# Optimization experiments

Hardware: AMD Instinct MI355X
Metric: run time of the kernel (lower is better)

Reference implementation:

```python
import jax, jax.numpy as jnp
import numpy as np


def setup_inputs() -> dict:
    key = jax.random.key(0)
    ks = jax.random.split(key, 6)
    B, C, H, W, K = 4, 64, 352, 1216, 3
    OC = K * K - 1  # 8 guide channels from convbn
    return {
        "feature": jax.random.normal(ks[0], (B, C, H, W), jnp.float32),
        "conv_w": jax.random.normal(ks[1], (OC, C, 3, 3), jnp.float32) * 0.05,
        "gamma": jax.random.uniform(ks[2], (OC,), jnp.float32, 0.5, 1.5),
        "beta": jax.random.normal(ks[3], (OC,), jnp.float32) * 0.1,
        "mean": jax.random.normal(ks[4], (OC,), jnp.float32) * 0.1,
        "var": jax.random.uniform(ks[5], (OC,), jnp.float32, 0.5, 1.5),
        "kernel_size": K,
    }


def reference(feature, conv_w, gamma, beta, mean, var, kernel_size):
    k = kernel_size
    eps = 1e-5
    # conv 3x3, stride 1, pad 1, no bias  -> [B, k*k-1, H, W]
    x = jax.lax.conv_general_dilated(
        feature, conv_w, window_strides=(1, 1), padding=((1, 1), (1, 1)),
        dimension_numbers=("NCHW", "OIHW", "NCHW"))
    c = lambda v: v[None, :, None, None]
    # BatchNorm2d in eval mode (running stats + affine)
    guide = (x - c(mean)) * (c(gamma) * jax.lax.rsqrt(c(var) + eps)) + c(beta)
    # L1-normalize across channels, middle weight = 1 - sum of the others
    gsum = jnp.sum(jnp.abs(guide), axis=1, keepdims=True)
    guide = guide / gsum
    guide_mid = 1.0 - jnp.sum(guide, axis=1, keepdims=True)
    mid = (k * k - 1) // 2
    # per-offset zero-pad each single channel into [H+k-1, W+k-1] canvas
    pads = []
    for t in range(k * k):  # fixed small loop over kernel offsets (k*k = 9)
        i, j = t // k, t % k  # top=i, bottom=k-1-i, left=j, right=k-1-j
        if t < mid:
            ch = guide[:, t:t + 1]
        elif t > mid:
            ch = guide[:, t - 1:t]
        else:
            ch = guide_mid
        pads.append(jnp.pad(ch, ((0, 0), (0, 0), (i, k - 1 - i), (j, k - 1 - j))))
    return jnp.concatenate(pads, axis=1)  # [B, k*k, H+k-1, W+k-1]
```

## Files before the change

### kernel.cpp

```cpp
#include <hip/hip_runtime.h>
#include <hip/hip_bf16.h>

#define BATCH 4
#define CIN 64
#define HH 352
#define WW 1216
#define OCH 8
#define OHH 354
#define OWW 1218
#define HW (HH * WW)

#define BH 16
#define BW 32
#define FR 18
#define FC 34
#define NPOS (FR * FC)
#define NTHR 256
#define NTASK (NPOS * 4)
#define NIT 10

typedef short bf16x8 __attribute__((ext_vector_type(8)));
typedef float f32x4  __attribute__((ext_vector_type(4)));

static __device__ __forceinline__ unsigned f2bf(float x) {
    unsigned u = __float_as_uint(x);
    return (u + 0x7FFFu + ((u >> 16) & 1u)) >> 16;
}

__global__ void repack_kernel(const float* __restrict__ conv_w,
                              const float* __restrict__ gamma,
                              const float* __restrict__ beta,
                              const float* __restrict__ mean,
                              const float* __restrict__ var,
                              unsigned short* __restrict__ wB,
                              float* __restrict__ bias)
{
    int tid = blockIdx.x * 256 + threadIdx.x;
    if (tid < 18 * 64) {
        int tc = tid >> 6;
        int lane = tid & 63;
        int tap = tc >> 1, cc = tc & 1;
        int oc = lane & 15, hi = lane >> 4;
        unsigned v[8];
#pragma unroll
        for (int j = 0; j < 8; ++j) {
            float w = 0.f;
            if (oc < 8) {
                int c = cc * 32 + hi * 8 + j;
                float scl = gamma[oc] * rsqrtf(var[oc] + 1e-5f);
                w = conv_w[((size_t)oc * CIN + c) * 9 + tap] * scl;
            }
            v[j] = f2bf(w);
        }
        uint4 pk;
        pk.x = v[0] | (v[1] << 16);
        pk.y = v[2] | (v[3] << 16);
        pk.z = v[4] | (v[5] << 16);
        pk.w = v[6] | (v[7] << 16);
        ((uint4*)wB)[tid] = pk;
    }
    if (tid < OCH) {
        float scl = gamma[tid] * rsqrtf(var[tid] + 1e-5f);
        bias[tid] = beta[tid] - mean[tid] * scl;
    }
}

__global__ void border_kernel(float* __restrict__ out)
{
    const int bt = blockIdx.x;
    const int t = bt % 9;
    const int i = t / 3, j = t % 3;
    float* pl = out + (size_t)bt * OHH * OWW;
    const int r0 = (i == 0) ? HH : 0;
    const int r1 = (i == 2) ? 1 : (OHH - 1);
    const int c0 = (j == 0) ? WW : 0;
    const int c1 = (j == 2) ? 1 : (OWW - 1);
    const int nrow = 2 * OWW;
    for (int idx = threadIdx.x; idx < 2 * OWW + 2 * OHH; idx += blockDim.x) {
        if (idx < nrow) {
            int r = (idx < OWW) ? r0 : r1;
            int c = (idx < OWW) ? idx : idx - OWW;
            pl[(size_t)r * OWW + c] = 0.f;
        } else {
            int k = idx - nrow;
            int c = (k < OHH) ? c0 : c1;
            int r = (k < OHH) ? k : k - OHH;
            pl[(size_t)r * OWW + c] = 0.f;
        }
    }
}

__global__ __launch_bounds__(NTHR, 2)
void conv_mfma(const float* __restrict__ feature,
               const unsigned short* __restrict__ wB,
               const float* __restrict__ bias,
               float* __restrict__ out)
{
    __shared__ uint4 sF[NPOS * 4];

    const int tid  = threadIdx.x;
    const int wave = tid >> 6;
    const int lane = tid & 63;
    const int oc   = lane & 15;
    const int hi   = lane >> 4;
    const int b  = blockIdx.z;
    const int h0 = blockIdx.y * BH;
    const int w0 = blockIdx.x * BW;

    const float* fb = feature + (size_t)b * CIN * HW;

    const int soct = tid & 3;
    const int p0   = tid >> 2;

    f32x4 acc[4][2];
#pragma unroll
    for (int rr = 0; rr < 4; ++rr)
#pragma unroll
        for (int cg = 0; cg < 2; ++cg) acc[rr][cg] = (f32x4)0.f;

#pragma unroll 1
    for (int cc = 0; cc < 2; ++cc) {
        if (cc) __syncthreads();

        const float* chbase = fb + (size_t)(cc * 32 + soct * 8) * HW;
        float v[NIT][8];
        float msk[NIT];
        int   cps[NIT];
#pragma unroll
        for (int it = 0; it < NIT; ++it) {
            int pos = p0 + it * 64;
            int cp = (pos < NPOS) ? pos : (NPOS - 1);
            int fr = cp / FC;
            int fc = cp - fr * FC;
            int gh = h0 - 1 + fr, gw = w0 - 1 + fc;
            bool ok = ((unsigned)gh < (unsigned)HH) && ((unsigned)gw < (unsigned)WW);
            int sgh = min(max(gh, 0), HH - 1);
            int sgw = min(max(gw, 0), WW - 1);
            const float* sp = chbase + sgh * WW + sgw;
#pragma unroll
            for (int j = 0; j < 8; ++j) v[it][j] = sp[(size_t)j * HW];
            msk[it] = ok ? 1.f : 0.f;
            cps[it] = cp;
        }
        bf16x8 bw[9];
#pragma unroll
        for (int t = 0; t < 9; ++t)
            bw[t] = ((const bf16x8*)wB)[(t * 2 + cc) * 64 + lane];
#pragma unroll
        for (int it = 0; it < NIT; ++it) {
            float mk = msk[it];
            uint4 pk;
            pk.x = f2bf(v[it][0] * mk) | (f2bf(v[it][1] * mk) << 16);
            pk.y = f2bf(v[it][2] * mk) | (f2bf(v[it][3] * mk) << 16);
            pk.z = f2bf(v[it][4] * mk) | (f2bf(v[it][5] * mk) << 16);
            pk.w = f2bf(v[it][6] * mk) | (f2bf(v[it][7] * mk) << 16);
            int cp = cps[it];
            sF[cp * 4 + (soct ^ ((cp >> 1) & 3))] = pk;
        }
        __syncthreads();

#pragma unroll
        for (int t = 0; t < 9; ++t) {
            const int dh = t / 3, dw = t % 3;
#pragma unroll
            for (int rr = 0; rr < 4; ++rr) {
                const int fr = wave * 4 + rr + dh;
#pragma unroll
                for (int cg = 0; cg < 2; ++cg) {
                    const int fc = cg * 16 + oc + dw;
                    const int pp = fr * FC + fc;
                    bf16x8 av = *reinterpret_cast<const bf16x8*>(&sF[pp * 4 + (hi ^ ((pp >> 1) & 3))]);
                    acc[rr][cg] = __builtin_amdgcn_mfma_f32_16x16x32_bf16(av, bw[t], acc[rr][cg], 0, 0, 0);
                }
            }
        }
    }

    const float myb = (oc < 8) ? bias[oc] : 0.f;
    const int t = (oc < 8) ? ((oc < 4) ? oc : oc + 1) : 4;
    const bool dow = (oc <= 8);
    const int ii = t / 3, jj = t % 3;
    float* pl = out + ((size_t)(b * 9 + t) * OHH + ii) * OWW + jj;

#pragma unroll
    for (int rr = 0; rr < 4; ++rr) {
        const int h = h0 + wave * 4 + rr;
#pragma unroll
        for (int cg = 0; cg < 2; ++cg) {
#pragma unroll
            for (int reg = 0; reg < 4; ++reg) {
                float v = acc[rr][cg][reg] + myb;
                float av = fabsf(v);
                float sv = v;
                av += __shfl_xor(av, 1);  sv += __shfl_xor(sv, 1);
                av += __shfl_xor(av, 2);  sv += __shfl_xor(sv, 2);
                av += __shfl_xor(av, 4);  sv += __shfl_xor(sv, 4);
                av += __shfl_xor(av, 8);  sv += __shfl_xor(sv, 8);
                float inv = 1.0f / av;
                float val = (oc == 8) ? (1.0f - sv * inv) : (v * inv);
                if (dow) {
                    int w = w0 + cg * 16 + hi * 4 + reg;
                    pl[(size_t)h * OWW + w] = val;
                }
            }
        }
    }
}

extern "C" void kernel_launch(void* const* d_in, const int* in_sizes, int n_in,
                              void* d_out, int out_size, void* d_ws, size_t ws_size,
                              hipStream_t stream) {
    const float* feature = (const float*)d_in[0];
    const float* conv_w  = (const float*)d_in[1];
    const float* gamma   = (const float*)d_in[2];
    const float* beta    = (const float*)d_in[3];
    const float* mean    = (const float*)d_in[4];
    const float* var     = (const float*)d_in[5];
    float* out = (float*)d_out;
    unsigned short* wB = (unsigned short*)d_ws;
    float* bias = (float*)((char*)d_ws + 18432);

    border_kernel<<<BATCH * 9, 256, 0, stream>>>(out);
    repack_kernel<<<5, 256, 0, stream>>>(conv_w, gamma, beta, mean, var, wB, bias);

    dim3 grid(WW / BW, HH / BH, BATCH);
    conv_mfma<<<grid, NTHR, 0, stream>>>(feature, wB, bias, out);
}
```

Before: 261.0 us.

## Pre-transpose feature to padded NHWC bf16 and read conv operands directly

Adds a transpose kernel that converts the NCHW fp32 feature map into a zero-padded NHWC bf16 buffer in workspace, plus a ring kernel that zeroes the padding border. The conv kernel then loads MFMA A operands straight from global memory as contiguous 16-byte channel vectors. This removes the LDS staging, the per-position masking and the strided per-channel loads. The cost is an extra full pass over the input (read fp32, write bf16) and dependence on workspace size; if the workspace is too small, the old path runs instead.

```diff
diff --git a/kernel.cpp b/kernel.cpp
--- a/kernel.cpp
+++ b/kernel.cpp
@@ -9,6 +9,8 @@
 #define OHH 354
 #define OWW 1218
 #define HW (HH * WW)
+#define HP 354
+#define WP 1218
 
 #define BH 16
 #define BW 32
@@ -16,8 +18,8 @@
 #define FC 34
 #define NPOS (FR * FC)
 #define NTHR 256
-#define NTASK (NPOS * 4)
 #define NIT 10
+#define NRING 3140
 
 typedef short bf16x8 __attribute__((ext_vector_type(8)));
 typedef float f32x4  __attribute__((ext_vector_type(4)));
@@ -90,14 +92,60 @@
     }
 }
 
+__global__ void ring_kernel(unsigned short* __restrict__ ft)
+{
+    int idx = blockIdx.x * 256 + threadIdx.x;
+    if (idx >= BATCH * NRING * 8) return;
+    int q = idx & 7;
+    int pp = idx >> 3;
+    int b = pp / NRING;
+    int r = pp - b * NRING;
+    int hp, wp;
+    if (r < WP)            { hp = 0;               wp = r; }
+    else if (r < 2 * WP)   { hp = HP - 1;          wp = r - WP; }
+    else if (r < 2 * WP + HH) { hp = 1 + (r - 2 * WP);      wp = 0; }
+    else                   { hp = 1 + (r - 2 * WP - HH);    wp = WP - 1; }
+    uint4 z; z.x = 0; z.y = 0; z.z = 0; z.w = 0;
+    *(uint4*)(ft + ((((size_t)b * HP + hp) * WP + wp) * 64 + q * 8)) = z;
+}
+
+__global__ __launch_bounds__(256, 2)
+void transpose_kernel(const float* __restrict__ feature,
+                      unsigned short* __restrict__ ft)
+{
+    __shared__ unsigned short sT[64 * 72];
+    const int tid = threadIdx.x;
+    const int tx = tid & 15, ty = tid >> 4;
+    const int w0 = blockIdx.x * 64;
+    const int h  = blockIdx.y;
+    const int b  = blockIdx.z;
+
+    const float* fb = feature + (size_t)b * CIN * HW + (size_t)h * WW + w0;
+#pragma unroll
+    for (int i = 0; i < 4; ++i) {
+        int ch = ty + i * 16;
+        float4 v = *(const float4*)(fb + (size_t)ch * HW + tx * 4);
+        int px = tx * 4;
+        sT[(px + 0) * 72 + ch] = (unsigned short)f2bf(v.x);
+        sT[(px + 1) * 72 + ch] = (unsigned short)f2bf(v.y);
+        sT[(px + 2) * 72 + ch] = (unsigned short)f2bf(v.z);
+        sT[(px + 3) * 72 + ch] = (unsigned short)f2bf(v.w);
+    }
+    __syncthreads();
+    const int pix = tid >> 2, q = tid & 3;
+    const uint4* src = (const uint4*)(sT + pix * 72 + q * 16);
+    unsigned short* dst = ft + ((((size_t)b * HP + (h + 1)) * WP + (w0 + pix + 1)) * 64 + q * 16);
+    uint4 a0 = src[0], a1 = src[1];
+    ((uint4*)dst)[0] = a0;
+    ((uint4*)dst)[1] = a1;
+}
+
 __global__ __launch_bounds__(NTHR, 2)
-void conv_mfma(const float* __restrict__ feature,
+void conv_nhwc(const unsigned short* __restrict__ ft,
                const unsigned short* __restrict__ wB,
                const float* __restrict__ bias,
                float* __restrict__ out)
 {
-    __shared__ uint4 sF[NPOS * 4];
-
     const int tid  = threadIdx.x;
     const int wave = tid >> 6;
     const int lane = tid & 63;
@@ -107,10 +155,10 @@
     const int h0 = blockIdx.y * BH;
     const int w0 = blockIdx.x * BW;
 
-    const float* fb = feature + (size_t)b * CIN * HW;
-
-    const int soct = tid & 3;
-    const int p0   = tid >> 2;
+    bf16x8 bw[18];
+#pragma unroll
+    for (int k = 0; k < 18; ++k)
+        bw[k] = ((const bf16x8*)wB)[k * 64 + lane];
 
     f32x4 acc[4][2];
 #pragma unroll
@@ -118,59 +166,22 @@
 #pragma unroll
         for (int cg = 0; cg < 2; ++cg) acc[rr][cg] = (f32x4)0.f;
 
-#pragma unroll 1
-    for (int cc = 0; cc < 2; ++cc) {
-        if (cc) __syncthreads();
-
-        const float* chbase = fb + (size_t)(cc * 32 + soct * 8) * HW;
-        float v[NIT][8];
-        float msk[NIT];
-        int   cps[NIT];
-#pragma unroll
-        for (int it = 0; it < NIT; ++it) {
-            int pos = p0 + it * 64;
-            int cp = (pos < NPOS) ? pos : (NPOS - 1);
-            int fr = cp / FC;
-            int fc = cp - fr * FC;
-            int gh = h0 - 1 + fr, gw = w0 - 1 + fc;
-            bool ok = ((unsigned)gh < (unsigned)HH) && ((unsigned)gw < (unsigned)WW);
-            int sgh = min(max(gh, 0), HH - 1);
-            int sgw = min(max(gw, 0), WW - 1);
-            const float* sp = chbase + sgh * WW + sgw;
-#pragma unroll
-            for (int j = 0; j < 8; ++j) v[it][j] = sp[(size_t)j * HW];
-            msk[it] = ok ? 1.f : 0.f;
-            cps[it] = cp;
-        }
-        bf16x8 bw[9];
-#pragma unroll
-        for (int t = 0; t < 9; ++t)
-            bw[t] = ((const bf16x8*)wB)[(t * 2 + cc) * 64 + lane];
-#pragma unroll
-        for (int it = 0; it < NIT; ++it) {
-            float mk = msk[it];
-            uint4 pk;
-            pk.x = f2bf(v[it][0] * mk) | (f2bf(v[it][1] * mk) << 16);
-            pk.y = f2bf(v[it][2] * mk) | (f2bf(v[it][3] * mk) << 16);
-            pk.z = f2bf(v[it][4] * mk) | (f2bf(v[it][5] * mk) << 16);
-            pk.w = f2bf(v[it][6] * mk) | (f2bf(v[it][7] * mk) << 16);
-            int cp = cps[it];
-            sF[cp * 4 + (soct ^ ((cp >> 1) & 3))] = pk;
-        }
-        __syncthreads();
-
+    const unsigned short* fbase = ft + (size_t)b * HP * WP * 64 + hi * 8;
+
+#pragma unroll
+    for (int rr = 0; rr < 4; ++rr) {
+        const int hrow = h0 + wave * 4 + rr;
 #pragma unroll
         for (int t = 0; t < 9; ++t) {
             const int dh = t / 3, dw = t % 3;
 #pragma unroll
-            for (int rr = 0; rr < 4; ++rr) {
-                const int fr = wave * 4 + rr + dh;
-#pragma unroll
-                for (int cg = 0; cg < 2; ++cg) {
-                    const int fc = cg * 16 + oc + dw;
-                    const int pp = fr * FC + fc;
-                    bf16x8 av = *reinterpret_cast<const bf16x8*>(&sF[pp * 4 + (hi ^ ((pp >> 1) & 3))]);
-                    acc[rr][cg] = __builtin_amdgcn_mfma_f32_16x16x32_bf16(av, bw[t], acc[rr][cg], 0, 0, 0);
+            for (int cg = 0; cg < 2; ++cg) {
+                const unsigned short* p =
+                    fbase + ((size_t)(hrow + dh) * WP + (w0 + oc + dw + cg * 16)) * 64;
+#pragma unroll
+                for (int cc = 0; cc < 2; ++cc) {
+                    bf16x8 av = *(const bf16x8*)(p + cc * 32);
+                    acc[rr][cg] = __builtin_amdgcn_mfma_f32_16x16x32_bf16(av, bw[t * 2 + cc], acc[rr][cg], 0, 0, 0);
                 }
             }
         }
@@ -207,6 +218,120 @@
     }
 }
 
+__global__ __launch_bounds__(NTHR, 2)
+void conv_mfma(const float* __restrict__ feature,
+               const unsigned short* __restrict__ wB,
+               const float* __restrict__ bias,
+               float* __restrict__ out)
+{
+    __shared__ uint4 sF[NPOS * 4];
+
+    const int tid  = threadIdx.x;
+    const int wave = tid >> 6;
+    const int lane = tid & 63;
+    const int oc   = lane & 15;
+    const int hi   = lane >> 4;
+    const int b  = blockIdx.z;
+    const int h0 = blockIdx.y * BH;
+    const int w0 = blockIdx.x * BW;
+
+    const float* fb = feature + (size_t)b * CIN * HW;
+    const int soct = tid & 3;
+    const int p0   = tid >> 2;
+
+    f32x4 acc[4][2];
+#pragma unroll
+    for (int rr = 0; rr < 4; ++rr)
+#pragma unroll
+        for (int cg = 0; cg < 2; ++cg) acc[rr][cg] = (f32x4)0.f;
+
+#pragma unroll 1
+    for (int cc = 0; cc < 2; ++cc) {
+        if (cc) __syncthreads();
+        const float* chbase = fb + (size_t)(cc * 32 + soct * 8) * HW;
+        float v[NIT][8];
+        float msk[NIT];
+        int   cps[NIT];
+#pragma unroll
+        for (int it = 0; it < NIT; ++it) {
+            int pos = p0 + it * 64;
+            int cp = (pos < NPOS) ? pos : (NPOS - 1);
+            int fr = cp / FC;
+            int fc = cp - fr * FC;
+            int gh = h0 - 1 + fr, gw = w0 - 1 + fc;
+            bool ok = ((unsigned)gh < (unsigned)HH) && ((unsigned)gw < (unsigned)WW);
+            int sgh = min(max(gh, 0), HH - 1);
+            int sgw = min(max(gw, 0), WW - 1);
+            const float* sp = chbase + sgh * WW + sgw;
+#pragma unroll
+            for (int j = 0; j < 8; ++j) v[it][j] = sp[(size_t)j * HW];
+            msk[it] = ok ? 1.f : 0.f;
+            cps[it] = cp;
+        }
+        bf16x8 bwl[9];
+#pragma unroll
+        for (int t = 0; t < 9; ++t)
+            bwl[t] = ((const bf16x8*)wB)[(t * 2 + cc) * 64 + lane];
+#pragma unroll
+        for (int it = 0; it < NIT; ++it) {
+            float mk = msk[it];
+            uint4 pk;
+            pk.x = f2bf(v[it][0] * mk) | (f2bf(v[it][1] * mk) << 16);
+            pk.y = f2bf(v[it][2] * mk) | (f2bf(v[it][3] * mk) << 16);
+            pk.z = f2bf(v[it][4] * mk) | (f2bf(v[it][5] * mk) << 16);
+            pk.w = f2bf(v[it][6] * mk) | (f2bf(v[it][7] * mk) << 16);
+            int cp = cps[it];
+            sF[cp * 4 + (soct ^ ((cp >> 1) & 3))] = pk;
+        }
+        __syncthreads();
+#pragma unroll
+        for (int t = 0; t < 9; ++t) {
+            const int dh = t / 3, dw = t % 3;
+#pragma unroll
+            for (int rr = 0; rr < 4; ++rr) {
+                const int fr = wave * 4 + rr + dh;
+#pragma unroll
+                for (int cg = 0; cg < 2; ++cg) {
+                    const int fc = cg * 16 + oc + dw;
+                    const int pp = fr * FC + fc;
+                    bf16x8 av = *reinterpret_cast<const bf16x8*>(&sF[pp * 4 + (hi ^ ((pp >> 1) & 3))]);
+                    acc[rr][cg] = __builtin_amdgcn_mfma_f32_16x16x32_bf16(av, bwl[t], acc[rr][cg], 0, 0, 0);
+                }
+            }
+        }
+    }
+
+    const float myb = (oc < 8) ? bias[oc] : 0.f;
+    const int t = (oc < 8) ? ((oc < 4) ? oc : oc + 1) : 4;
+    const bool dow = (oc <= 8);
+    const int ii = t / 3, jj = t % 3;
+    float* pl = out + ((size_t)(b * 9 + t) * OHH + ii) * OWW + jj;
+
+#pragma unroll
+    for (int rr = 0; rr < 4; ++rr) {
+        const int h = h0 + wave * 4 + rr;
+#pragma unroll
+        for (int cg = 0; cg < 2; ++cg) {
+#pragma unroll
+            for (int reg = 0; reg < 4; ++reg) {
+                float v = acc[rr][cg][reg] + myb;
+                float av = fabsf(v);
+                float sv = v;
+                av += __shfl_xor(av, 1);  sv += __shfl_xor(sv, 1);
+                av += __shfl_xor(av, 2);  sv += __shfl_xor(sv, 2);
+                av += __shfl_xor(av, 4);  sv += __shfl_xor(sv, 4);
+                av += __shfl_xor(av, 8);  sv += __shfl_xor(sv, 8);
+                float inv = 1.0f / av;
+                float val = (oc == 8) ? (1.0f - sv * inv) : (v * inv);
+                if (dow) {
+                    int w = w0 + cg * 16 + hi * 4 + reg;
+                    pl[(size_t)h * OWW + w] = val;
+                }
+            }
+        }
+    }
+}
+
 extern "C" void kernel_launch(void* const* d_in, const int* in_sizes, int n_in,
                               void* d_out, int out_size, void* d_ws, size_t ws_size,
                               hipStream_t stream) {
@@ -217,12 +342,23 @@
     const float* mean    = (const float*)d_in[4];
     const float* var     = (const float*)d_in[5];
     float* out = (float*)d_out;
+
     unsigned short* wB = (unsigned short*)d_ws;
     float* bias = (float*)((char*)d_ws + 18432);
+    unsigned short* ft = (unsigned short*)((char*)d_ws + 32768);
+    const size_t ft_bytes = (size_t)BATCH * HP * WP * 64 * 2;
+    const size_t need = 32768 + ft_bytes;
 
     border_kernel<<<BATCH * 9, 256, 0, stream>>>(out);
     repack_kernel<<<5, 256, 0, stream>>>(conv_w, gamma, beta, mean, var, wB, bias);
 
     dim3 grid(WW / BW, HH / BH, BATCH);
-    conv_mfma<<<grid, NTHR, 0, stream>>>(feature, wB, bias, out);
-}
+
+    if (ws_size >= need) {
+        ring_kernel<<<(BATCH * NRING * 8 + 255) / 256, 256, 0, stream>>>(ft);
+        transpose_kernel<<<dim3(WW / 64, HH, BATCH), 256, 0, stream>>>(feature, ft);
+        conv_nhwc<<<grid, NTHR, 0, stream>>>(ft, wB, bias, out);
+    } else {
+        conv_mfma<<<grid, NTHR, 0, stream>>>(feature, wB, bias, out);
+    }
+}
```

Measured after the change: 326.5 us. 1.25x slower.

## Double-buffer channel chunks in LDS and remap blocks across XCDs

Applied to the files above, without the earlier changes.

Splits the shared-memory tile into two buffers so the global loads for the second 32-channel chunk are issued before the MFMA work on the first chunk, overlapping memory latency with compute. All 18 weight fragments and the per-position offsets and masks are computed once up front. The 3D grid becomes a 1D grid with a remapping that gives each XCD a contiguous range of tiles, aiming to improve L2 locality for the halo rows. Costs are doubled LDS per block and more registers, which may reduce occupancy.

```diff
diff --git a/kernel.cpp b/kernel.cpp
--- a/kernel.cpp
+++ b/kernel.cpp
@@ -16,8 +16,11 @@
 #define FC 34
 #define NPOS (FR * FC)
 #define NTHR 256
-#define NTASK (NPOS * 4)
 #define NIT 10
+#define GX 38
+#define GY 22
+#define NWG (GX * GY * BATCH)
+#define CPX (NWG / 8)
 
 typedef short bf16x8 __attribute__((ext_vector_type(8)));
 typedef float f32x4  __attribute__((ext_vector_type(4)));
@@ -90,91 +93,104 @@
     }
 }
 
+#define ISSUE(VB, CC) { \
+    const float* chb = fb + (size_t)((CC) * 32 + soct * 8) * HW; \
+    _Pragma("unroll") for (int it = 0; it < NIT; ++it) { \
+        const float* sp = chb + off[it]; \
+        _Pragma("unroll") for (int j = 0; j < 8; ++j) VB[it][j] = sp[(size_t)j * HW]; \
+    } }
+
+#define PACK(VB, BUF) { \
+    _Pragma("unroll") for (int it = 0; it < NIT; ++it) { \
+        float mk = msk[it]; \
+        uint4 pk; \
+        pk.x = f2bf(VB[it][0] * mk) | (f2bf(VB[it][1] * mk) << 16); \
+        pk.y = f2bf(VB[it][2] * mk) | (f2bf(VB[it][3] * mk) << 16); \
+        pk.z = f2bf(VB[it][4] * mk) | (f2bf(VB[it][5] * mk) << 16); \
+        pk.w = f2bf(VB[it][6] * mk) | (f2bf(VB[it][7] * mk) << 16); \
+        (BUF)[slot[it]] = pk; \
+    } }
+
+#define MFMA_CHUNK(BUF, CC) \
+    _Pragma("unroll") for (int t = 0; t < 9; ++t) { \
+        const int dh = t / 3, dw = t % 3; \
+        _Pragma("unroll") for (int rr = 0; rr < 4; ++rr) { \
+            const int frq = wv4 + rr + dh; \
+            _Pragma("unroll") for (int cg = 0; cg < 2; ++cg) { \
+                const int fcq = cg * 16 + oc + dw; \
+                const int pp = frq * FC + fcq; \
+                bf16x8 av = *reinterpret_cast<const bf16x8*>(&(BUF)[pp * 4 + (hi ^ ((pp >> 1) & 3))]); \
+                acc[rr][cg] = __builtin_amdgcn_mfma_f32_16x16x32_bf16(av, bw[t * 2 + (CC)], acc[rr][cg], 0, 0, 0); \
+            } } }
+
 __global__ __launch_bounds__(NTHR, 2)
 void conv_mfma(const float* __restrict__ feature,
                const unsigned short* __restrict__ wB,
                const float* __restrict__ bias,
                float* __restrict__ out)
 {
-    __shared__ uint4 sF[NPOS * 4];
+    __shared__ uint4 sA[NPOS * 4];
+    __shared__ uint4 sB[NPOS * 4];
+
+    const int lin = blockIdx.x;
+    const int wg  = (lin & 7) * CPX + (lin >> 3);
+    const int bx  = wg % GX;
+    const int byz = wg / GX;
+    const int by  = byz % GY;
+    const int b   = byz / GY;
 
     const int tid  = threadIdx.x;
     const int wave = tid >> 6;
     const int lane = tid & 63;
     const int oc   = lane & 15;
     const int hi   = lane >> 4;
-    const int b  = blockIdx.z;
-    const int h0 = blockIdx.y * BH;
-    const int w0 = blockIdx.x * BW;
+    const int wv4  = wave * 4;
+    const int h0 = by * BH;
+    const int w0 = bx * BW;
 
     const float* fb = feature + (size_t)b * CIN * HW;
-
     const int soct = tid & 3;
     const int p0   = tid >> 2;
 
+    int   off[NIT], slot[NIT];
+    float msk[NIT];
+#pragma unroll
+    for (int it = 0; it < NIT; ++it) {
+        int pos = p0 + it * 64;
+        int cp = (pos < NPOS) ? pos : (NPOS - 1);
+        int fr = cp / FC;
+        int fc = cp - fr * FC;
+        int gh = h0 - 1 + fr, gw = w0 - 1 + fc;
+        bool ok = ((unsigned)gh < (unsigned)HH) && ((unsigned)gw < (unsigned)WW);
+        int sgh = min(max(gh, 0), HH - 1);
+        int sgw = min(max(gw, 0), WW - 1);
+        off[it]  = sgh * WW + sgw;
+        msk[it]  = ok ? 1.f : 0.f;
+        slot[it] = cp * 4 + (soct ^ ((cp >> 1) & 3));
+    }
+
     f32x4 acc[4][2];
 #pragma unroll
     for (int rr = 0; rr < 4; ++rr)
 #pragma unroll
         for (int cg = 0; cg < 2; ++cg) acc[rr][cg] = (f32x4)0.f;
 
-#pragma unroll 1
-    for (int cc = 0; cc < 2; ++cc) {
-        if (cc) __syncthreads();
-
-        const float* chbase = fb + (size_t)(cc * 32 + soct * 8) * HW;
-        float v[NIT][8];
-        float msk[NIT];
-        int   cps[NIT];
-#pragma unroll
-        for (int it = 0; it < NIT; ++it) {
-            int pos = p0 + it * 64;
-            int cp = (pos < NPOS) ? pos : (NPOS - 1);
-            int fr = cp / FC;
-            int fc = cp - fr * FC;
-            int gh = h0 - 1 + fr, gw = w0 - 1 + fc;
-            bool ok = ((unsigned)gh < (unsigned)HH) && ((unsigned)gw < (unsigned)WW);
-            int sgh = min(max(gh, 0), HH - 1);
-            int sgw = min(max(gw, 0), WW - 1);
-            const float* sp = chbase + sgh * WW + sgw;
-#pragma unroll
-            for (int j = 0; j < 8; ++j) v[it][j] = sp[(size_t)j * HW];
-            msk[it] = ok ? 1.f : 0.f;
-            cps[it] = cp;
-        }
-        bf16x8 bw[9];
-#pragma unroll
-        for (int t = 0; t < 9; ++t)
-            bw[t] = ((const bf16x8*)wB)[(t * 2 + cc) * 64 + lane];
-#pragma unroll
-        for (int it = 0; it < NIT; ++it) {
-            float mk = msk[it];
-            uint4 pk;
-            pk.x = f2bf(v[it][0] * mk) | (f2bf(v[it][1] * mk) << 16);
-            pk.y = f2bf(v[it][2] * mk) | (f2bf(v[it][3] * mk) << 16);
-            pk.z = f2bf(v[it][4] * mk) | (f2bf(v[it][5] * mk) << 16);
-            pk.w = f2bf(v[it][6] * mk) | (f2bf(v[it][7] * mk) << 16);
-            int cp = cps[it];
-            sF[cp * 4 + (soct ^ ((cp >> 1) & 3))] = pk;
-        }
-        __syncthreads();
-
-#pragma unroll
-        for (int t = 0; t < 9; ++t) {
-            const int dh = t / 3, dw = t % 3;
-#pragma unroll
-            for (int rr = 0; rr < 4; ++rr) {
-                const int fr = wave * 4 + rr + dh;
-#pragma unroll
-                for (int cg = 0; cg < 2; ++cg) {
-                    const int fc = cg * 16 + oc + dw;
-                    const int pp = fr * FC + fc;
-                    bf16x8 av = *reinterpret_cast<const bf16x8*>(&sF[pp * 4 + (hi ^ ((pp >> 1) & 3))]);
-                    acc[rr][cg] = __builtin_amdgcn_mfma_f32_16x16x32_bf16(av, bw[t], acc[rr][cg], 0, 0, 0);
-                }
-            }
-        }
-    }
+    float v[NIT][8];
+
+    ISSUE(v, 0)
+    bf16x8 bw[18];
+#pragma unroll
+    for (int k = 0; k < 18; ++k)
+        bw[k] = ((const bf16x8*)wB)[k * 64 + lane];
+    PACK(v, sA)
+    __syncthreads();
+
+    ISSUE(v, 1)
+    __builtin_amdgcn_sched_barrier(0);
+    MFMA_CHUNK(sA, 0)
+    PACK(v, sB)
+    __syncthreads();
+    MFMA_CHUNK(sB, 1)
 
     const float myb = (oc < 8) ? bias[oc] : 0.f;
     const int t = (oc < 8) ? ((oc < 4) ? oc : oc + 1) : 4;
@@ -184,20 +200,20 @@
 
 #pragma unroll
     for (int rr = 0; rr < 4; ++rr) {
-        const int h = h0 + wave * 4 + rr;
+        const int h = h0 + wv4 + rr;
 #pragma unroll
         for (int cg = 0; cg < 2; ++cg) {
 #pragma unroll
             for (int reg = 0; reg < 4; ++reg) {
-                float v = acc[rr][cg][reg] + myb;
-                float av = fabsf(v);
-                float sv = v;
+                float vv = acc[rr][cg][reg] + myb;
+                float av = fabsf(vv);
+                float sv = vv;
                 av += __shfl_xor(av, 1);  sv += __shfl_xor(sv, 1);
                 av += __shfl_xor(av, 2);  sv += __shfl_xor(sv, 2);
                 av += __shfl_xor(av, 4);  sv += __shfl_xor(sv, 4);
                 av += __shfl_xor(av, 8);  sv += __shfl_xor(sv, 8);
                 float inv = 1.0f / av;
-                float val = (oc == 8) ? (1.0f - sv * inv) : (v * inv);
+                float val = (oc == 8) ? (1.0f - sv * inv) : (vv * inv);
                 if (dow) {
                     int w = w0 + cg * 16 + hi * 4 + reg;
                     pl[(size_t)h * OWW + w] = val;
@@ -217,12 +233,11 @@
     const float* mean    = (const float*)d_in[4];
     const float* var     = (const float*)d_in[5];
     float* out = (float*)d_out;
+
     unsigned short* wB = (unsigned short*)d_ws;
     float* bias = (float*)((char*)d_ws + 18432);
 
     border_kernel<<<BATCH * 9, 256, 0, stream>>>(out);
     repack_kernel<<<5, 256, 0, stream>>>(conv_w, gamma, beta, mean, var, wB, bias);
-
-    dim3 grid(WW / BW, HH / BH, BATCH);
-    conv_mfma<<<grid, NTHR, 0, stream>>>(feature, wB, bias, out);
-}
+    conv_mfma<<<NWG, NTHR, 0, stream>>>(feature, wB, bias, out);
+}
```

Measured after the change: 288.4 us. 10.5% more time.
